# Optimization experiments

Hardware: AMD Instinct MI355X
Metric: run time of the kernel (lower is better)

## Reference

```python
import jax, jax.numpy as jnp
import numpy as np

HIDDEN = 1024
HEADS = 16
DEPTH = HIDDEN // HEADS  # 64
B, S = 1, 2048  # batch must be 1: E is built with shape (heads, B*S, depth) and the skew reshape assumes B*S == S


def setup_inputs() -> dict:
    key = jax.random.key(0)
    ks = jax.random.split(key, 6)
    std = 0.02
    x = jax.random.normal(ks[0], (B, S, HIDDEN), dtype=jnp.float32)
    c_attn_w = jax.random.normal(ks[1], (HIDDEN, 3 * HIDDEN), dtype=jnp.float32) * std
    c_attn_b = jnp.zeros((1, 3 * HIDDEN), dtype=jnp.float32)
    c_proj_w = jax.random.normal(ks[2], (HIDDEN, HIDDEN), dtype=jnp.float32) * std
    c_proj_b = jnp.zeros((1, HIDDEN), dtype=jnp.float32)
    # GlorotUniform for E of shape (heads, B*S, depth)
    limit = float(np.sqrt(6.0 / (B * S + DEPTH)))
    E = jax.random.uniform(ks[3], (HEADS, B * S, DEPTH), dtype=jnp.float32,
                           minval=-limit, maxval=limit)
    return {"x": x, "c_attn_w": c_attn_w, "c_attn_b": c_attn_b,
            "c_proj_w": c_proj_w, "c_proj_b": c_proj_b, "E": E}


def _split_heads(t):
    # [B,S,H] -> [B,heads,S,depth]
    b, s, h = t.shape
    return t.reshape(b, s, HEADS, h // HEADS).transpose(0, 2, 1, 3)


def _relative_attention(q, E):
    # Transformer-XL style skewing. q: [B,heads,S,depth], E: [heads,B*S,depth]
    b, h, s, d = q.shape
    q_ = q.transpose(1, 0, 2, 3).reshape(h, b * s, d)
    rel = jnp.einsum('hnd,hmd->hnm', q_, E)            # [h, B*S, B*S]
    rel = rel.reshape(h, b, s, s)
    rel = jnp.pad(rel, ((0, 0), (0, 0), (0, 0), (1, 0)))  # pad left on last dim
    rel = rel.reshape(h, b, s + 1, s)[:, :, 1:]            # skew
    return rel.transpose(1, 0, 2, 3)                       # [B,heads,S,S]


def reference(x, c_attn_w, c_attn_b, c_proj_w, c_proj_b, E):
    b, s, hidden = x.shape
    qkv = x @ c_attn_w + c_attn_b                      # [B,S,3H]
    q, k, v = jnp.split(qkv, 3, axis=2)
    q, k, v = _split_heads(q), _split_heads(k), _split_heads(v)  # [B,h,S,d]

    w = jnp.einsum('bhqd,bhkd->bhqk', q, k)            # raw scores
    w = w + _relative_attention(q, E)
    w = w * jax.lax.rsqrt(jnp.asarray(DEPTH, w.dtype))  # scale applied after rel bias

    # causal mask: 1 in lower triangle (i >= j - ns + nd, nd == ns == S)
    i = jnp.arange(s)[:, None]
    j = jnp.arange(s)[None, :]
    bmask = (i >= j).astype(w.dtype)[None, None]        # [1,1,S,S]
    w = w * bmask - 10000.0 * (1.0 - bmask)

    a = jax.nn.softmax(w, axis=-1)                      # dropout is identity at inference
    ctx = jnp.einsum('bhqk,bhkd->bhqd', a, v)
    ctx = ctx.transpose(0, 2, 1, 3).reshape(b, s, hidden)  # merge heads
    out = ctx @ c_proj_w + c_proj_b
    return out
```

## Files before the change

### kernel.cpp

```cpp
#include <hip/hip_runtime.h>
#include <math.h>

#define SEQ  2048
#define NH   16
#define DEP  64
#define HID  1024

typedef __attribute__((ext_vector_type(8))) short s16x8;
typedef __attribute__((ext_vector_type(4))) float f32x4;

#define MFMA16(a, b, c) __builtin_amdgcn_mfma_f32_16x16x32_bf16(a, b, c, 0, 0, 0)
#define GLDS16(g, l)                                                           \
  __builtin_amdgcn_global_load_lds(                                            \
      (const __attribute__((address_space(1))) void*)(g),                      \
      (__attribute__((address_space(3))) void*)(l), 16, 0, 0)

__device__ __forceinline__ ushort f2b(float f) {
  union { float f; unsigned u; } x; x.f = f;
  unsigned r = (x.u + 0x7fff + ((x.u >> 16) & 1)) >> 16;
  return (ushort)r;
}
__device__ __forceinline__ float b2f(ushort u) {
  union { unsigned u; float f; } x; x.u = ((unsigned)u) << 16;
  return x.f;
}

__global__ __launch_bounds__(256) void prep(
    const float* __restrict__ x, ushort* __restrict__ xb,
    const float* __restrict__ E, ushort* __restrict__ Eb,
    const float* __restrict__ Wa, ushort* __restrict__ Wat,
    const float* __restrict__ Wp, ushort* __restrict__ Wpt) {
  const int bid = blockIdx.x, t = threadIdx.x;
  if (bid < 1024) {
    __shared__ float Ls[64 * 68];
    const float* in; ushort* out; int C, tile;
    if (bid < 768) { in = Wa; out = Wat; C = 3072; tile = bid; }
    else           { in = Wp; out = Wpt; C = 1024; tile = bid - 768; }
    const int ntx = C / 64;
    const int n0 = (tile % ntx) * 64, k0 = (tile / ntx) * 64;
    const int r = t >> 4, c4 = t & 15;
    #pragma unroll
    for (int p = 0; p < 4; p++) {
      float4 v = *(const float4*)&in[(size_t)(k0 + r + 16 * p) * C + n0 + c4 * 4];
      *(float4*)&Ls[(r + 16 * p) * 68 + c4 * 4] = v;
    }
    __syncthreads();
    #pragma unroll
    for (int p = 0; p < 4; p++) {
      int rw = r + 16 * p;
      ushort4 o;
      o.x = f2b(Ls[(c4 * 4 + 0) * 68 + rw]);
      o.y = f2b(Ls[(c4 * 4 + 1) * 68 + rw]);
      o.z = f2b(Ls[(c4 * 4 + 2) * 68 + rw]);
      o.w = f2b(Ls[(c4 * 4 + 3) * 68 + rw]);
      *(ushort4*)&out[(size_t)(n0 + rw) * 1024 + k0 + c4 * 4] = o;
    }
  } else {
    const int id = bid - 1024;
    #pragma unroll
    for (int rep = 0; rep < 4; rep++) {
      int i = id * 256 + t + rep * 262144;
      const float* src; ushort* dst; int k;
      if (i < 524288) { src = x; dst = xb; k = i; }
      else            { src = E; dst = Eb; k = i - 524288; }
      float4 v = *(const float4*)&src[(size_t)k * 4];
      ushort4 o = {f2b(v.x), f2b(v.y), f2b(v.z), f2b(v.w)};
      *(ushort4*)&dst[(size_t)k * 4] = o;
    }
  }
}

__global__ __launch_bounds__(256, 3) void gemm_qkv(
    const ushort* __restrict__ A, const ushort* __restrict__ Bt,
    const float* __restrict__ bias, int N, int K,
    ushort* __restrict__ qd, ushort* __restrict__ kd, ushort* __restrict__ vt) {
  __shared__ ushort As[2][64 * 64];
  __shared__ ushort Bs[2][128 * 64];
  const int t = threadIdx.x, l = t & 63, w = t >> 6;
  const int lr = l & 15, quad = l >> 4;
  const int row8 = l >> 3;
  const int chunk = (l & 7) ^ ((l >> 3) & 7);
  const int m0 = blockIdx.y * 64, n0 = blockIdx.x * 128;
  const int wr = (w >> 1) * 32, wc = (w & 1) * 64;
  f32x4 acc[2][4] = {};
  const ushort* gA = A + (size_t)m0 * K + chunk * 8;
  const ushort* gB = Bt + (size_t)n0 * K + chunk * 8;

  auto issue = [&](int buf, int k0) {
    #pragma unroll
    for (int g = 0; g < 2; g++) {
      int r = 16 * w + 8 * g + row8;
      GLDS16(gA + (size_t)r * K + k0, &As[buf][(16 * w + 8 * g) * 64]);
    }
    #pragma unroll
    for (int g = 0; g < 4; g++) {
      int r = 32 * w + 8 * g + row8;
      GLDS16(gB + (size_t)r * K + k0, &Bs[buf][(32 * w + 8 * g) * 64]);
    }
  };

  issue(0, 0);
  const int nsteps = K / 64;
  for (int s = 0; s < nsteps; s++) {
    __syncthreads();
    if (s + 1 < nsteps) issue((s + 1) & 1, (s + 1) * 64);
    const char* as_ = (const char*)As[s & 1];
    const char* bs_ = (const char*)Bs[s & 1];
    s16x8 af[2][2], bf[4][2];
    #pragma unroll
    for (int i = 0; i < 2; i++)
      #pragma unroll
      for (int hh = 0; hh < 2; hh++)
        af[i][hh] = *(const s16x8*)(as_ + (wr + 16 * i + lr) * 128 +
                                    (((4 * hh + quad) ^ (lr & 7)) * 16));
    #pragma unroll
    for (int j = 0; j < 4; j++)
      #pragma unroll
      for (int hh = 0; hh < 2; hh++)
        bf[j][hh] = *(const s16x8*)(bs_ + (wc + 16 * j + lr) * 128 +
                                    (((4 * hh + quad) ^ (lr & 7)) * 16));
    #pragma unroll
    for (int i = 0; i < 2; i++)
      #pragma unroll
      for (int j = 0; j < 4; j++) {
        acc[i][j] = MFMA16(af[i][0], bf[j][0], acc[i][j]);
        acc[i][j] = MFMA16(af[i][1], bf[j][1], acc[i][j]);
      }
  }

  #pragma unroll
  for (int i = 0; i < 2; i++) {
    #pragma unroll
    for (int j = 0; j < 4; j++) {
      const int colg = n0 + wc + 16 * j + lr;
      const float bb = bias[colg];
      const int rowg0 = m0 + wr + 16 * i + 4 * quad;
      const int part = colg >> 10, hh = (colg >> 6) & 15, d = colg & 63;
      if (part == 2) {
        ushort4 ov;
        ov.x = f2b(acc[i][j][0] + bb);
        ov.y = f2b(acc[i][j][1] + bb);
        ov.z = f2b(acc[i][j][2] + bb);
        ov.w = f2b(acc[i][j][3] + bb);
        *(ushort4*)&vt[((size_t)hh * 64 + d) * SEQ + rowg0] = ov;
      } else {
        ushort* dst = part == 0 ? qd : kd;
        const float sc = part == 0 ? 0.125f : 1.0f;
        #pragma unroll
        for (int r = 0; r < 4; r++)
          dst[((size_t)hh * SEQ + rowg0 + r) * 64 + d] = f2b((acc[i][j][r] + bb) * sc);
      }
    }
  }
}

__global__ __launch_bounds__(256, 3) void gemm_proj(
    const ushort* __restrict__ A, const ushort* __restrict__ Bt,
    const float* __restrict__ bias, float* __restrict__ Cout) {
  const int K = HID, N = HID;
  __shared__ ushort As[2][64 * 64];
  __shared__ ushort Bs[2][64 * 64];
  const int t = threadIdx.x, l = t & 63, w = t >> 6;
  const int lr = l & 15, quad = l >> 4;
  const int row8 = l >> 3;
  const int chunk = (l & 7) ^ ((l >> 3) & 7);
  const int m0 = blockIdx.y * 64, n0 = blockIdx.x * 64;
  const int wr = (w >> 1) * 32, wc = (w & 1) * 32;
  f32x4 acc[2][2] = {};
  const ushort* gA = A + (size_t)m0 * K + chunk * 8;
  const ushort* gB = Bt + (size_t)n0 * K + chunk * 8;

  auto issue = [&](int buf, int k0) {
    #pragma unroll
    for (int g = 0; g < 2; g++) {
      int r = 16 * w + 8 * g;
      GLDS16(gA + (size_t)(r + row8) * K + k0, &As[buf][r * 64]);
      GLDS16(gB + (size_t)(r + row8) * K + k0, &Bs[buf][r * 64]);
    }
  };

  issue(0, 0);
  const int nsteps = K / 64;
  for (int s = 0; s < nsteps; s++) {
    __syncthreads();
    if (s + 1 < nsteps) issue((s + 1) & 1, (s + 1) * 64);
    const char* as_ = (const char*)As[s & 1];
    const char* bs_ = (const char*)Bs[s & 1];
    s16x8 af[2][2], bf[2][2];
    #pragma unroll
    for (int i = 0; i < 2; i++)
      #pragma unroll
      for (int hh = 0; hh < 2; hh++)
        af[i][hh] = *(const s16x8*)(as_ + (wr + 16 * i + lr) * 128 +
                                    (((4 * hh + quad) ^ (lr & 7)) * 16));
    #pragma unroll
    for (int j = 0; j < 2; j++)
      #pragma unroll
      for (int hh = 0; hh < 2; hh++)
        bf[j][hh] = *(const s16x8*)(bs_ + (wc + 16 * j + lr) * 128 +
                                    (((4 * hh + quad) ^ (lr & 7)) * 16));
    #pragma unroll
    for (int i = 0; i < 2; i++)
      #pragma unroll
      for (int j = 0; j < 2; j++) {
        acc[i][j] = MFMA16(af[i][0], bf[j][0], acc[i][j]);
        acc[i][j] = MFMA16(af[i][1], bf[j][1], acc[i][j]);
      }
  }

  #pragma unroll
  for (int i = 0; i < 2; i++)
    #pragma unroll
    for (int j = 0; j < 2; j++) {
      const int colg = n0 + wc + 16 * j + lr;
      const float bb = bias[colg];
      const int rowg0 = m0 + wr + 16 * i + 4 * quad;
      #pragma unroll
      for (int r = 0; r < 4; r++)
        Cout[(size_t)(rowg0 + r) * N + colg] = acc[i][j][r] + bb;
    }
}

__global__ __launch_bounds__(256, 2) void attn_mfma(
    const ushort* __restrict__ qw, const ushort* __restrict__ kw,
    const ushort* __restrict__ vT, const ushort* __restrict__ Ebf,
    ushort* __restrict__ ctx, ushort* __restrict__ pa_o,
    float* __restrict__ pa_l) {
  __shared__ ushort KT[2][64 * 64];
  __shared__ ushort EB[4][64 * 64];
  __shared__ ushort PB[4][16 * 72];
  const int t = threadIdx.x, l = t & 63, w = t >> 6;
  const int lr = l & 15, quad = l >> 4;
  const int row8 = l >> 3;
  const int chunk = (l & 7) ^ ((l >> 3) & 7);
  const int h = blockIdx.y;
  const int p = blockIdx.x >> 1, half = blockIdx.x & 1;
  const int i0A = 64 * p, i0B = 64 * (31 - p);

  int ph_i0[2], ph_k0[2], ph_k1[2], nph, tot;
  bool ph_diag[2], ph_dir[2];
  if (half == 0) {
    ph_i0[0] = i0A; ph_k0[0] = 0; ph_k1[0] = p + 1;  ph_diag[0] = true;  ph_dir[0] = true;
    ph_i0[1] = i0B; ph_k0[1] = 0; ph_k1[1] = 16 - p; ph_diag[1] = false; ph_dir[1] = false;
    nph = 2; tot = 17;
  } else {
    ph_i0[0] = i0B; ph_k0[0] = 16 - p; ph_k1[0] = 32 - p; ph_diag[0] = true; ph_dir[0] = false;
    ph_i0[1] = 0; ph_k0[1] = 0; ph_k1[1] = 0; ph_diag[1] = false; ph_dir[1] = false;
    nph = 1; tot = 16;
  }

  const ushort* kwh = kw + (size_t)h * SEQ * 64;
  const ushort* vgh = vT + (size_t)h * 64 * SEQ;
  const ushort* egh = Ebf + (size_t)h * SEQ * 64;

  auto issue_k = [&](int buf, int j0) {
    const ushort* kb = kwh + (size_t)j0 * 64 + chunk * 8;
    #pragma unroll
    for (int g = 0; g < 2; g++) {
      int r = 16 * w + 8 * g + row8;
      GLDS16(kb + (size_t)r * 64, &KT[buf][(16 * w + 8 * g) * 64]);
    }
  };
  auto issue_e = [&](int slot, int r0) {
    #pragma unroll
    for (int g = 0; g < 2; g++) {
      int r = r0 + 16 * w + 8 * g + row8;
      if (r > SEQ - 1) r = SEQ - 1;
      GLDS16(egh + (size_t)r * 64 + chunk * 8, &EB[slot][(16 * w + 8 * g) * 64]);
    }
  };

  int pi = 0, kt = ph_k0[0], ebs = 0;
  {
    const int m0 = 1984 - ph_i0[0] + kt * 64;
    issue_k(0, kt * 64);
    issue_e(0, m0);
    issue_e(1, m0 + 64);
  }

  s16x8 aq0, aq1;
  {
    const ushort* qg = qw + ((size_t)h * SEQ + ph_i0[0] + 16 * w) * 64;
    aq0 = *(const s16x8*)(qg + lr * 64 + quad * 8);
    aq1 = *(const s16x8*)(qg + lr * 64 + 32 + quad * 8);
  }

  f32x4 o[4] = {};
  float li[4] = {0.f, 0.f, 0.f, 0.f};
  f32x4 rtc = {};

  for (int s = 0; s < tot; s++) {
    __syncthreads();

    const int i0 = ph_i0[pi];
    const bool first = (kt == ph_k0[pi]);
    const bool last = (kt == ph_k1[pi] - 1);
    const bool diag = ph_diag[pi] && last;
    const int j0 = kt * 64;

    s16x8 vv[4][2];
    #pragma unroll
    for (int dc = 0; dc < 4; dc++) {
      const ushort* vr = vgh + (size_t)(16 * dc + lr) * SEQ + j0 + quad * 8;
      vv[dc][0] = *(const s16x8*)vr;
      vv[dc][1] = *(const s16x8*)(vr + 32);
    }

    int ebs_next = ebs;
    {
      int npi = pi, nkt = kt + 1;
      bool have = true, newph = false;
      if (nkt == ph_k1[pi]) {
        if (pi + 1 < nph) { npi = pi + 1; nkt = ph_k0[npi]; newph = true; }
        else have = false;
      }
      if (have) {
        issue_k((s + 1) & 1, nkt * 64);
        const int m0n = 1984 - ph_i0[npi] + nkt * 64;
        if (newph) {
          issue_e((ebs + 2) & 3, m0n);
          issue_e((ebs + 3) & 3, m0n + 64);
          ebs_next = (ebs + 2) & 3;
        } else {
          issue_e((ebs + 2) & 3, m0n + 64);
          ebs_next = (ebs + 1) & 3;
        }
      }
    }

    const char* KTc = (const char*)KT[s & 1];

    auto eb_frag = [&](int row, s16x8& e0, s16x8& e1) {
      const char* e_ = (const char*)EB[(ebs + (row >> 6)) & 3];
      const int rb = (row & 63) * 128;
      e0 = *(const s16x8*)(e_ + rb + ((quad ^ (lr & 7)) * 16));
      e1 = *(const s16x8*)(e_ + rb + (((4 + quad) ^ (lr & 7)) * 16));
    };

    f32x4 s4[4];
    __builtin_amdgcn_s_setprio(1);
    #pragma unroll
    for (int b = 0; b < 4; b++) {
      const int row = 16 * b + lr;
      s16x8 bk0 = *(const s16x8*)(KTc + row * 128 + ((quad ^ (lr & 7)) * 16));
      s16x8 bk1 = *(const s16x8*)(KTc + row * 128 + (((4 + quad) ^ (lr & 7)) * 16));
      f32x4 z = {};
      z = MFMA16(aq0, bk0, z);
      z = MFMA16(aq1, bk1, z);
      s4[b] = z;
    }
    __builtin_amdgcn_s_setprio(0);

    {
      const int ebase = 48 - 16 * w;
      f32x4 rt[5];
      __builtin_amdgcn_s_setprio(1);
      if (first) {
        s16x8 e0, e1;
        eb_frag(ebase + lr, e0, e1);
        f32x4 z = {};
        z = MFMA16(aq0, e0, z);
        z = MFMA16(aq1, e1, z);
        rt[0] = z;
      } else {
        rt[0] = rtc;
      }
      #pragma unroll
      for (int b = 1; b < 5; b++) {
        s16x8 e0, e1;
        eb_frag(ebase + 16 * b + lr, e0, e1);
        f32x4 z = {};
        z = MFMA16(aq0, e0, z);
        z = MFMA16(aq1, e1, z);
        rt[b] = z;
      }
      __builtin_amdgcn_s_setprio(0);
      rtc = rt[4];
      #pragma unroll
      for (int r = 0; r < 4; r++) {
        const int ti = 4 * quad + r;
        const int u = lr - ti + 15;
        const int src = (u & 15) | (l & 48);
        const float sh0 = __shfl(rt[0][r], src);
        const float sh1 = __shfl(rt[1][r], src);
        const float sh2 = __shfl(rt[2][r], src);
        const float sh3 = __shfl(rt[3][r], src);
        const float sh4 = __shfl(rt[4][r], src);
        s4[0][r] += (u < 16) ? sh0 : sh1;
        s4[1][r] += (u < 16) ? sh1 : sh2;
        s4[2][r] += (u < 16) ? sh2 : sh3;
        s4[3][r] += (u < 16) ? sh3 : sh4;
      }
    }

    if (diag) {
      #pragma unroll
      for (int b = 0; b < 4; b++)
        #pragma unroll
        for (int r = 0; r < 4; r++) {
          int ii = 16 * w + 4 * quad + r;
          if (16 * b + lr > ii) s4[b][r] = -10000.0f;
        }
    }

    #pragma unroll
    for (int b = 0; b < 4; b++)
      #pragma unroll
      for (int r = 0; r < 4; r++) {
        float pp = __expf(s4[b][r]);
        s4[b][r] = pp;
        li[r] += pp;
      }

    {
      char* Pw = (char*)PB[w];
      #pragma unroll
      for (int b = 0; b < 4; b++)
        #pragma unroll
        for (int r = 0; r < 4; r++)
          *(ushort*)(Pw + (4 * quad + r) * 144 + (16 * b + lr) * 2) = f2b(s4[b][r]);
      s16x8 pa0 = *(const s16x8*)(Pw + lr * 144 + quad * 16);
      s16x8 pa1 = *(const s16x8*)(Pw + lr * 144 + 64 + quad * 16);
      __builtin_amdgcn_s_setprio(1);
      #pragma unroll
      for (int dc = 0; dc < 4; dc++) {
        o[dc] = MFMA16(pa0, vv[dc][0], o[dc]);
        o[dc] = MFMA16(pa1, vv[dc][1], o[dc]);
      }
      __builtin_amdgcn_s_setprio(0);
    }

    if (last) {
      float lsum[4];
      #pragma unroll
      for (int r = 0; r < 4; r++) {
        float v = li[r];
        v += __shfl_xor(v, 1);
        v += __shfl_xor(v, 2);
        v += __shfl_xor(v, 4);
        v += __shfl_xor(v, 8);
        lsum[r] = v;
      }
      if (ph_dir[pi]) {
        #pragma unroll
        for (int r = 0; r < 4; r++) {
          float inv = 1.0f / lsum[r];
          #pragma unroll
          for (int dc = 0; dc < 4; dc++) {
            int row = i0 + 16 * w + 4 * quad + r;
            int col = h * 64 + 16 * dc + lr;
            ctx[(size_t)row * HID + col] = f2b(o[dc][r] * inv);
          }
        }
      } else {
        ushort* po = pa_o + (((size_t)(h * 16 + p) * 2 + half) * 4096);
        float* pl = pa_l + (((size_t)(h * 16 + p) * 2 + half) * 64);
        #pragma unroll
        for (int r = 0; r < 4; r++) {
          int row = 16 * w + 4 * quad + r;
          #pragma unroll
          for (int dc = 0; dc < 4; dc++)
            po[row * 64 + 16 * dc + lr] = f2b(o[dc][r]);
          if (lr == 0) pl[row] = lsum[r];
        }
      }
      #pragma unroll
      for (int dc = 0; dc < 4; dc++) o[dc] = (f32x4){0.f, 0.f, 0.f, 0.f};
      #pragma unroll
      for (int r = 0; r < 4; r++) li[r] = 0.f;
      if (pi + 1 < nph) {
        const ushort* qg = qw + ((size_t)h * SEQ + ph_i0[pi + 1] + 16 * w) * 64;
        aq0 = *(const s16x8*)(qg + lr * 64 + quad * 8);
        aq1 = *(const s16x8*)(qg + lr * 64 + 32 + quad * 8);
      }
    }

    if (kt + 1 == ph_k1[pi]) { pi++; kt = (pi < nph) ? ph_k0[pi] : 0; }
    else kt++;
    ebs = ebs_next;
  }
}

__global__ __launch_bounds__(256) void merge_p(const ushort* __restrict__ pa_o,
                                               const float* __restrict__ pa_l,
                                               ushort* __restrict__ ctx) {
  const int p = blockIdx.x, h = blockIdx.y, t = threadIdx.x;
  const int row = t >> 2, seg = t & 3;
  const ushort* o0 = pa_o + ((size_t)(h * 16 + p) * 2 + 0) * 4096;
  const ushort* o1 = pa_o + ((size_t)(h * 16 + p) * 2 + 1) * 4096;
  const float* l0 = pa_l + ((size_t)(h * 16 + p) * 2 + 0) * 64;
  const float* l1 = pa_l + ((size_t)(h * 16 + p) * 2 + 1) * 64;
  const float inv = 1.0f / (l0[row] + l1[row]);
  const int i0b = 64 * (31 - p);
  #pragma unroll
  for (int g = 0; g < 2; g++) {
    ushort a[8], b[8], r[8];
    *(int4*)a = *(const int4*)&o0[row * 64 + seg * 16 + g * 8];
    *(int4*)b = *(const int4*)&o1[row * 64 + seg * 16 + g * 8];
    #pragma unroll
    for (int j = 0; j < 8; j++) r[j] = f2b((b2f(a[j]) + b2f(b[j])) * inv);
    *(int4*)&ctx[(size_t)(i0b + row) * HID + h * 64 + seg * 16 + g * 8] = *(int4*)r;
  }
}

extern "C" void kernel_launch(void* const* d_in, const int* in_sizes, int n_in,
                              void* d_out, int out_size, void* d_ws, size_t ws_size,
                              hipStream_t stream) {
  (void)in_sizes; (void)n_in; (void)out_size; (void)ws_size;
  const float* x  = (const float*)d_in[0];
  const float* Wa = (const float*)d_in[1];
  const float* ba = (const float*)d_in[2];
  const float* Wp = (const float*)d_in[3];
  const float* bp = (const float*)d_in[4];
  const float* E  = (const float*)d_in[5];
  float* out = (float*)d_out;

  ushort* xb  = (ushort*)d_ws;
  ushort* ctx = xb;
  ushort* Wat = xb + (size_t)2 * 1024 * 1024;
  ushort* Wpt = Wat + (size_t)3 * 1024 * 1024;
  ushort* Ebf = Wpt + (size_t)1024 * 1024;
  ushort* qwp = Ebf + (size_t)2 * 1024 * 1024;
  ushort* kwp = qwp + (size_t)2 * 1024 * 1024;
  ushort* vTp = kwp + (size_t)2 * 1024 * 1024;
  ushort* pa_o = Wat;
  float*  pa_l = (float*)(Wat + (size_t)2 * 1024 * 1024);

  prep<<<2048, 256, 0, stream>>>(x, xb, E, Ebf, Wa, Wat, Wp, Wpt);
  gemm_qkv<<<dim3(24, 32), 256, 0, stream>>>(xb, Wat, ba, 3 * HID, HID,
                                             qwp, kwp, vTp);
  attn_mfma<<<dim3(32, NH), 256, 0, stream>>>(qwp, kwp, vTp, Ebf, ctx,
                                              pa_o, pa_l);
  merge_p<<<dim3(16, NH), 256, 0, stream>>>(pa_o, pa_l, ctx);
  gemm_proj<<<dim3(16, 32), 256, 0, stream>>>(ctx, Wpt, bp, out);
}
```

Before: 167.2 us.

## Stage V tiles through LDS with async loads and remap blocks across XCDs

V tiles are now fetched with global_load_lds into a double-buffered LDS array alongside K, prefetched one step ahead, and read back with swizzled LDS reads, replacing synchronous per-wave global loads in the loop. The grid becomes 1D with a head mapping that interleaves blocks so each XCD handles a pair of heads, aiming at better L2 reuse of K/V/E per head. The s_setprio hints around the MFMA sections are also removed. This adds 16 KB of LDS per block, which may limit occupancy.

Measured after the change: 158.7 us, median of 2. 1.05x faster.

```diff
diff --git a/kernel.cpp b/kernel.cpp
--- a/kernel.cpp
+++ b/kernel.cpp
@@ -227,14 +227,17 @@
     ushort* __restrict__ ctx, ushort* __restrict__ pa_o,
     float* __restrict__ pa_l) {
   __shared__ ushort KT[2][64 * 64];
+  __shared__ ushort VS[2][64 * 64];
   __shared__ ushort EB[4][64 * 64];
   __shared__ ushort PB[4][16 * 72];
   const int t = threadIdx.x, l = t & 63, w = t >> 6;
   const int lr = l & 15, quad = l >> 4;
   const int row8 = l >> 3;
   const int chunk = (l & 7) ^ ((l >> 3) & 7);
-  const int h = blockIdx.y;
-  const int p = blockIdx.x >> 1, half = blockIdx.x & 1;
+  const int bid = blockIdx.x;
+  const int h = (bid & 7) * 2 + ((bid >> 3) >> 5);
+  const int s32 = (bid >> 3) & 31;
+  const int p = s32 >> 1, half = s32 & 1;
   const int i0A = 64 * p, i0B = 64 * (31 - p);
 
   int ph_i0[2], ph_k0[2], ph_k1[2], nph, tot;
@@ -253,12 +256,14 @@
   const ushort* vgh = vT + (size_t)h * 64 * SEQ;
   const ushort* egh = Ebf + (size_t)h * SEQ * 64;
 
-  auto issue_k = [&](int buf, int j0) {
+  auto issue_kv = [&](int buf, int j0) {
     const ushort* kb = kwh + (size_t)j0 * 64 + chunk * 8;
+    const ushort* vb = vgh + j0 + chunk * 8;
     #pragma unroll
     for (int g = 0; g < 2; g++) {
       int r = 16 * w + 8 * g + row8;
       GLDS16(kb + (size_t)r * 64, &KT[buf][(16 * w + 8 * g) * 64]);
+      GLDS16(vb + (size_t)r * SEQ, &VS[buf][(16 * w + 8 * g) * 64]);
     }
   };
   auto issue_e = [&](int slot, int r0) {
@@ -273,7 +278,7 @@
   int pi = 0, kt = ph_k0[0], ebs = 0;
   {
     const int m0 = 1984 - ph_i0[0] + kt * 64;
-    issue_k(0, kt * 64);
+    issue_kv(0, kt * 64);
     issue_e(0, m0);
     issue_e(1, m0 + 64);
   }
@@ -296,15 +301,6 @@
     const bool first = (kt == ph_k0[pi]);
     const bool last = (kt == ph_k1[pi] - 1);
     const bool diag = ph_diag[pi] && last;
-    const int j0 = kt * 64;
-
-    s16x8 vv[4][2];
-    #pragma unroll
-    for (int dc = 0; dc < 4; dc++) {
-      const ushort* vr = vgh + (size_t)(16 * dc + lr) * SEQ + j0 + quad * 8;
-      vv[dc][0] = *(const s16x8*)vr;
-      vv[dc][1] = *(const s16x8*)(vr + 32);
-    }
 
     int ebs_next = ebs;
     {
@@ -315,7 +311,7 @@
         else have = false;
       }
       if (have) {
-        issue_k((s + 1) & 1, nkt * 64);
+        issue_kv((s + 1) & 1, nkt * 64);
         const int m0n = 1984 - ph_i0[npi] + nkt * 64;
         if (newph) {
           issue_e((ebs + 2) & 3, m0n);
@@ -329,6 +325,7 @@
     }
 
     const char* KTc = (const char*)KT[s & 1];
+    const char* VSc = (const char*)VS[s & 1];
 
     auto eb_frag = [&](int row, s16x8& e0, s16x8& e1) {
       const char* e_ = (const char*)EB[(ebs + (row >> 6)) & 3];
@@ -338,7 +335,6 @@
     };
 
     f32x4 s4[4];
-    __builtin_amdgcn_s_setprio(1);
     #pragma unroll
     for (int b = 0; b < 4; b++) {
       const int row = 16 * b + lr;
@@ -349,12 +345,10 @@
       z = MFMA16(aq1, bk1, z);
       s4[b] = z;
     }
-    __builtin_amdgcn_s_setprio(0);
 
     {
       const int ebase = 48 - 16 * w;
       f32x4 rt[5];
-      __builtin_amdgcn_s_setprio(1);
       if (first) {
         s16x8 e0, e1;
         eb_frag(ebase + lr, e0, e1);
@@ -374,7 +368,6 @@
         z = MFMA16(aq1, e1, z);
         rt[b] = z;
       }
-      __builtin_amdgcn_s_setprio(0);
       rtc = rt[4];
       #pragma unroll
       for (int r = 0; r < 4; r++) {
@@ -421,13 +414,14 @@
           *(ushort*)(Pw + (4 * quad + r) * 144 + (16 * b + lr) * 2) = f2b(s4[b][r]);
       s16x8 pa0 = *(const s16x8*)(Pw + lr * 144 + quad * 16);
       s16x8 pa1 = *(const s16x8*)(Pw + lr * 144 + 64 + quad * 16);
-      __builtin_amdgcn_s_setprio(1);
       #pragma unroll
       for (int dc = 0; dc < 4; dc++) {
-        o[dc] = MFMA16(pa0, vv[dc][0], o[dc]);
-        o[dc] = MFMA16(pa1, vv[dc][1], o[dc]);
-      }
-      __builtin_amdgcn_s_setprio(0);
+        const int row = 16 * dc + lr;
+        s16x8 bv0 = *(const s16x8*)(VSc + row * 128 + ((quad ^ (lr & 7)) * 16));
+        s16x8 bv1 = *(const s16x8*)(VSc + row * 128 + (((4 + quad) ^ (lr & 7)) * 16));
+        o[dc] = MFMA16(pa0, bv0, o[dc]);
+        o[dc] = MFMA16(pa1, bv1, o[dc]);
+      }
     }
 
     if (last) {
@@ -529,8 +523,7 @@
   prep<<<2048, 256, 0, stream>>>(x, xb, E, Ebf, Wa, Wat, Wp, Wpt);
   gemm_qkv<<<dim3(24, 32), 256, 0, stream>>>(xb, Wat, ba, 3 * HID, HID,
                                              qwp, kwp, vTp);
-  attn_mfma<<<dim3(32, NH), 256, 0, stream>>>(qwp, kwp, vTp, Ebf, ctx,
-                                              pa_o, pa_l);
+  attn_mfma<<<512, 256, 0, stream>>>(qwp, kwp, vTp, Ebf, ctx, pa_o, pa_l);
   merge_p<<<dim3(16, NH), 256, 0, stream>>>(pa_o, pa_l, ctx);
   gemm_proj<<<dim3(16, 32), 256, 0, stream>>>(ctx, Wpt, bp, out);
 }
```
